# Kernel optimization log

Hardware: AMD Instinct MI355X
Metric: run time of the kernel (lower is better)

## Reference

```python
import jax, jax.numpy as jnp
import numpy as np

E = 20    # number of residue types (rc.restypes)
NB = 2    # num_blocks per AngleHead
NA = 7    # num_angles
C_S = 384
C_H = 128
BS, L = 8, 2048


def setup_inputs() -> dict:
    key = jax.random.key(0)
    ks = jax.random.split(key, 16)
    sc = 0.02
    return {
        "s": jax.random.normal(ks[0], (BS, L, C_S), dtype=jnp.float32),
        "s_init": jax.random.normal(ks[1], (BS, L, C_S), dtype=jnp.float32),
        "aatype": jax.random.randint(ks[2], (BS, L), 0, E, dtype=jnp.int32),
        # stacked per-residue-type AngleHead params
        "Win": jax.random.normal(ks[3], (E, C_S, C_H), dtype=jnp.float32) * sc,
        "b_in": jax.random.normal(ks[4], (E, C_H), dtype=jnp.float32) * sc,
        "Winit": jax.random.normal(ks[5], (E, C_S, C_H), dtype=jnp.float32) * sc,
        "b_init2": jax.random.normal(ks[6], (E, C_H), dtype=jnp.float32) * sc,
        "Wb1": jax.random.normal(ks[7], (E, NB, C_H, C_H), dtype=jnp.float32) * sc,
        "bb1": jax.random.normal(ks[8], (E, NB, C_H), dtype=jnp.float32) * sc,
        "Wb2": jax.random.normal(ks[9], (E, NB, C_H, C_H), dtype=jnp.float32) * sc,
        "bb2": jax.random.normal(ks[10], (E, NB, C_H), dtype=jnp.float32) * sc,
        "Wout": jax.random.normal(ks[11], (E, C_H, NA * 2), dtype=jnp.float32) * sc,
        "b_out": jax.random.normal(ks[12], (E, NA * 2), dtype=jnp.float32) * sc,
    }


def reference(s, s_init, aatype, Win, b_in, Winit, b_init2, Wb1, bb1, Wb2, bb2, Wout, b_out):
    relu = jax.nn.relu
    bs, seq_len, c_s = s.shape
    N = bs * seq_len
    sf = s.reshape(N, c_s)          # [N, c_s]
    si = s_init.reshape(N, c_s)     # [N, c_s]

    # Dense dispatch: run every token through all E per-type heads, then
    # combine with the one-hot routing mask (math identical to the torch
    # gather/scatter loop over residue types).
    h = jnp.einsum('nd,edh->neh', relu(sf), Win) + b_in            # [N,E,H]
    h = h + jnp.einsum('nd,edh->neh', relu(si), Winit) + b_init2   # [N,E,H]

    for b in range(NB):  # ResidualBlock1d: s + W2 @ relu(W1 @ relu(s))
        a = jnp.einsum('neh,ehk->nek', relu(h), Wb1[:, b]) + bb1[:, b]
        a = jnp.einsum('nek,ekh->neh', relu(a), Wb2[:, b]) + bb2[:, b]
        h = h + a

    out = jnp.einsum('neh,eho->neo', relu(h), Wout) + b_out        # [N,E,2*NA]
    sel = jax.nn.one_hot(aatype.reshape(N), E, dtype=out.dtype)    # [N,E]
    ang = jnp.einsum('neo,ne->no', out, sel).reshape(bs, seq_len, NA, 2)

    # F.normalize(dim=-1): x / max(||x||, eps)
    nrm = jnp.maximum(jnp.linalg.norm(ang, axis=-1, keepdims=True), 1e-12)
    return ang / nrm
```

## Files before the change

kernel.cpp:

```cpp
#include <hip/hip_runtime.h>
#include <math.h>

#define E_TYPES 20
#define NBLK 2
#define NANG 7
#define CS 384
#define CH 128
#define N_TOK (8 * 2048)
#define TOK 32
#define TPB 256
#define TPB_MAIN 512
#define KC 128
#define MAX_TILES (N_TOK / TOK + E_TYPES)
#define NPREP 64

#define HIST_OFF 0

#define WT1_OFF (256 * 1024)
#define WT1_SZ  (20 * 8 * 24 * 2048)
#define WTR_OFF (WT1_OFF + WT1_SZ)

typedef __attribute__((ext_vector_type(8))) short bfrag;
typedef __attribute__((ext_vector_type(4))) float f32x4;
typedef unsigned short (*arr136)[136];

#define BAR() do { \
    asm volatile("s_waitcnt lgkmcnt(0)" ::: "memory"); \
    __builtin_amdgcn_s_barrier(); \
    asm volatile("" ::: "memory"); \
} while (0)

__device__ __forceinline__ void split_bf16(float x, unsigned short& h, unsigned short& l) {
    unsigned int u = __float_as_uint(x);
    unsigned int hb = (u + 0x7FFFu + ((u >> 16) & 1u)) & 0xFFFF0000u;
    h = (unsigned short)(hb >> 16);
    float r = x - __uint_as_float(hb);
    unsigned int v = __float_as_uint(r);
    l = (unsigned short)((v + 0x7FFFu + ((v >> 16) & 1u)) >> 16);
}

__global__ void prep1(const float* __restrict__ Win, const float* __restrict__ Winit,
                      const float* __restrict__ Wb1, const float* __restrict__ Wb2,
                      const int* __restrict__ aatype, int* __restrict__ wsI,
                      unsigned short* __restrict__ wt) {
    __shared__ int lh[E_TYPES];
    int bid = blockIdx.x;
    int t = threadIdx.x;
    if (bid >= 1600) {
        int b2 = bid - 1600;
        if (t < E_TYPES) lh[t] = 0;
        __syncthreads();
        int idx = b2 * 256 + t;
        if (idx < N_TOK) atomicAdd(&lh[aatype[idx]], 1);
        __syncthreads();
        if (t < E_TYPES) wsI[HIST_OFF + b2 * E_TYPES + t] = lh[t];
        return;
    }
    int gid = bid * 256 + t;
    unsigned short h[8], l[8];
    if (gid < 245760) {
        int lane = gid & 63;
        int bi = gid >> 6;
        int kb = bi % 24;
        int r = bi / 24;
        int nt = r & 7, e = r >> 3;
        int n = nt * 16 + (lane & 15);
        int k0 = kb * 32 + (lane >> 4) * 8;
        #pragma unroll
        for (int j = 0; j < 8; j++) {
            int k = k0 + j;
            float x = (k < CS) ? Win[((size_t)e * CS + k) * CH + n]
                               : Winit[((size_t)e * CS + (k - CS)) * CH + n];
            split_bf16(x, h[j], l[j]);
        }
        unsigned short* dst = wt + (WT1_OFF / 2) + (size_t)bi * 1024 + lane * 8;
        *(bfrag*)dst = *(bfrag*)h;
        *(bfrag*)(dst + 512) = *(bfrag*)l;
    } else {
        gid -= 245760;
        int lane = gid & 63;
        int bi = gid >> 6;
        int kb = bi & 3;
        int nt = (bi >> 2) & 7;
        int m4 = (bi >> 5) & 3;
        int e = bi >> 7;
        int b = m4 >> 1;
        const float* W = (m4 & 1) ? Wb2 : Wb1;
        int n = nt * 16 + (lane & 15);
        int k0 = kb * 32 + (lane >> 4) * 8;
        #pragma unroll
        for (int j = 0; j < 8; j++) {
            int k = k0 + j;
            float x = W[(((size_t)e * NBLK + b) * CH + k) * CH + n];
            split_bf16(x, h[j], l[j]);
        }
        unsigned short* dst = wt + (WTR_OFF / 2) + (size_t)bi * 1024 + lane * 8;
        *(bfrag*)dst = *(bfrag*)h;
        *(bfrag*)(dst + 512) = *(bfrag*)l;
    }
}

#define MFMA(a, b, c) __builtin_amdgcn_mfma_f32_16x16x32_bf16((a), (b), (c), 0, 0, 0)

__global__ __launch_bounds__(TPB_MAIN, 4)
void angle_main(const float* __restrict__ s, const float* __restrict__ si,
                const float* __restrict__ b_in, const float* __restrict__ b_init2,
                const float* __restrict__ bb1, const float* __restrict__ bb2,
                const float* __restrict__ Wout, const float* __restrict__ b_out,
                const int* __restrict__ aatype,
                const int* __restrict__ wsI, const unsigned short* __restrict__ wt,
                float* __restrict__ out)
{
    #define BUFSZ 17408
    __shared__ __align__(16) char pool[2 * BUFSZ];
    __shared__ int ptok[TOK];
    __shared__ int cntS[E_TYPES];

    arr136 AH0 = (arr136)(pool);
    arr136 AL0 = (arr136)(pool + 8704);
    arr136 AH1 = (arr136)(pool + BUFSZ);
    arr136 AL1 = (arr136)(pool + BUFSZ + 8704);
    float (*Hf)[132] = (float (*)[132])(pool);
    float (*Of)[16]  = (float (*)[16])(pool + BUFSZ);

    int t = threadIdx.x;
    int w = t >> 6, lane = t & 63;
    int lane15 = lane & 15, quad = lane >> 4;

    int bid = blockIdx.x;
    const int q = MAX_TILES >> 3, r = MAX_TILES & 7;
    int xcd = bid & 7, sub = bid >> 3;
    int tile = (xcd < r ? xcd * (q + 1) : r * (q + 1) + (xcd - r) * q) + sub;

    if (w == 0 && lane < E_TYPES) {
        int c = 0;
        #pragma unroll
        for (int b = 0; b < NPREP; b++) c += wsI[HIST_OFF + b * E_TYPES + lane];
        cntS[lane] = c;
    }
    BAR();

    int pos = tile * TOK;
    int e = -1, poff_e = 0;
    {
        int accT = 0;
        #pragma unroll
        for (int ee = 0; ee < E_TYPES; ee++) {
            int pad = (cntS[ee] + TOK - 1) & ~(TOK - 1);
            if (e < 0 && pos < accT + pad) { e = ee; poff_e = accT; }
            accT += pad;
        }
        if (pos >= accT) return;
    }
    int pos_in = pos - poff_e;
    int n = cntS[e] - pos_in; if (n > TOK) n = TOK;

    int nc = w * 16 + lane15;
    const bfrag* wt1 = (const bfrag*)((const char*)wt + WT1_OFF);
    const bfrag* wtr = (const bfrag*)((const char*)wt + WTR_OFF);
    size_t wb = (size_t)(e * 8 + w) * 24;

    bfrag Bd[2][4];
    {
        const bfrag* nb = wt1 + wb * 128 + lane;
        Bd[0][0] = nb[0];   Bd[0][1] = nb[128];
        Bd[0][2] = nb[64];  Bd[0][3] = nb[192];
    }
    float bv_in  = b_in[e * CH + nc] + b_init2[e * CH + nc];
    float bvb1a = bb1[(e * NBLK + 0) * CH + nc];
    float bvb1b = bb1[(e * NBLK + 1) * CH + nc];
    float bvb2a = bb2[(e * NBLK + 0) * CH + nc];
    float bvb2b = bb2[(e * NBLK + 1) * CH + nc];

    if (w == 0) {
        int hb = wsI[HIST_OFF + lane * E_TYPES + e];
        int inc = hb;
        #pragma unroll
        for (int d = 1; d < 64; d <<= 1) { int v = __shfl_up(inc, d); if (lane >= d) inc += v; }
        int pre = inc - hb;
        unsigned long long mle = __ballot(pre <= pos_in);
        int cb = 63 - __clzll(mle);
        int running = __shfl(pre, cb);
        int base = cb * 256;
        int lim = pos_in + n;
        while (running < lim && base < N_TOK) {
            const int4 a4 = *(const int4*)&aatype[base + lane * 4];
            int m0 = (a4.x == e), m1 = (a4.y == e), m2 = (a4.z == e), m3 = (a4.w == e);
            int c = m0 + m1 + m2 + m3;
            int incl = c;
            #pragma unroll
            for (int d = 1; d < 64; d <<= 1) { int v = __shfl_up(incl, d); if (lane >= d) incl += v; }
            int rk = running + incl - c;
            int tk = base + lane * 4;
            if (m0) { if (rk >= pos_in && rk < lim) ptok[rk - pos_in] = tk;     rk++; }
            if (m1) { if (rk >= pos_in && rk < lim) ptok[rk - pos_in] = tk + 1; rk++; }
            if (m2) { if (rk >= pos_in && rk < lim) ptok[rk - pos_in] = tk + 2; rk++; }
            if (m3) { if (rk >= pos_in && rk < lim) ptok[rk - pos_in] = tk + 3; rk++; }
            running += __shfl(incl, 63);
            base += 256;
        }
        int t0 = ptok[0];
        if (lane >= n && lane < TOK) ptok[lane] = t0;
    }
    BAR();

    int srow = t >> 4;
    int scol = (t & 15) * 8;
    size_t rowoff = (size_t)ptok[srow] * CS + scol;
    float4 p0 = *(const float4*)(s + rowoff);
    float4 p1 = *(const float4*)(s + rowoff + 4);
    {
        float xv[8] = {p0.x, p0.y, p0.z, p0.w, p1.x, p1.y, p1.z, p1.w};
        unsigned short h8[8], l8[8];
        #pragma unroll
        for (int j = 0; j < 8; j++) split_bf16(fmaxf(xv[j], 0.f), h8[j], l8[j]);
        *(bfrag*)&AH0[srow][scol] = *(bfrag*)h8;
        *(bfrag*)&AL0[srow][scol] = *(bfrag*)l8;
    }
    p0 = *(const float4*)(s + rowoff + KC);
    p1 = *(const float4*)(s + rowoff + KC + 4);

    f32x4 aA0 = (f32x4){bv_in, bv_in, bv_in, bv_in};
    f32x4 aA1 = aA0;
    f32x4 aB0 = (f32x4){0.f, 0.f, 0.f, 0.f};
    f32x4 aB1 = aB0;
    BAR();

    #pragma unroll
    for (int c = 0; c < 6; c++) {
        arr136 WAH = (c & 1) ? AH1 : AH0;
        arr136 WAL = (c & 1) ? AL1 : AL0;
        const bfrag* wbase = wt1 + (wb + c * 4) * 128 + lane;
        bfrag c2h = wbase[256], c2l = wbase[320];
        bfrag c3h = wbase[384], c3l = wbase[448];
        #pragma unroll
        for (int ks = 0; ks < 4; ks++) {
            bfrag bh = (ks == 0) ? Bd[c & 1][0] : (ks == 1) ? Bd[c & 1][1]
                      : (ks == 2) ? c2h : c3h;
            bfrag bl = (ks == 0) ? Bd[c & 1][2] : (ks == 1) ? Bd[c & 1][3]
                      : (ks == 2) ? c2l : c3l;
            int kl = ks * 32 + quad * 8;
            bfrag ah0 = *(const bfrag*)&WAH[lane15][kl];
            bfrag ah1 = *(const bfrag*)&WAH[16 + lane15][kl];
            bfrag al0 = *(const bfrag*)&WAL[lane15][kl];
            bfrag al1 = *(const bfrag*)&WAL[16 + lane15][kl];
            aA0 = MFMA(ah0, bh, aA0);
            aB0 = MFMA(ah0, bl, aB0);
            aB0 = MFMA(al0, bh, aB0);
            aA1 = MFMA(ah1, bh, aA1);
            aB1 = MFMA(ah1, bl, aB1);
            aB1 = MFMA(al1, bh, aB1);
            if (ks == 1) {
                const bfrag* nb = (c < 5)
                    ? wt1 + (wb + (c + 1) * 4) * 128 + lane
                    : wtr + ((size_t)(e * 4 + 0) * 8 + w) * 4 * 128 + lane;
                Bd[(c + 1) & 1][0] = nb[0];   Bd[(c + 1) & 1][1] = nb[128];
                Bd[(c + 1) & 1][2] = nb[64];  Bd[(c + 1) & 1][3] = nb[192];
            }
        }
        if (c < 5) {
            arr136 NH = (c & 1) ? AH0 : AH1;
            arr136 NL = (c & 1) ? AL0 : AL1;
            float xv[8] = {p0.x, p0.y, p0.z, p0.w, p1.x, p1.y, p1.z, p1.w};
            unsigned short h8[8], l8[8];
            #pragma unroll
            for (int j = 0; j < 8; j++) split_bf16(fmaxf(xv[j], 0.f), h8[j], l8[j]);
            *(bfrag*)&NH[srow][scol] = *(bfrag*)h8;
            *(bfrag*)&NL[srow][scol] = *(bfrag*)l8;
            if (c < 4) {
                const float* src = (c + 2 < 3) ? s : si;
                int kb0 = ((c + 2 < 3) ? (c + 2) : (c - 1)) * KC;
                p0 = *(const float4*)(src + rowoff + kb0);
                p1 = *(const float4*)(src + rowoff + kb0 + 4);
            }
        }
        BAR();
    }

    f32x4 h0 = aA0 + aB0;
    f32x4 h1 = aA1 + aB1;
    {
        f32x4 cur[2] = {h0, h1};
        #pragma unroll
        for (int mt = 0; mt < 2; mt++) {
            #pragma unroll
            for (int rr = 0; rr < 4; rr++) {
                unsigned short hh, ll;
                split_bf16(fmaxf(cur[mt][rr], 0.f), hh, ll);
                AH0[mt * 16 + quad * 4 + rr][nc] = hh;
                AL0[mt * 16 + quad * 4 + rr][nc] = ll;
            }
        }
    }
    BAR();

    #pragma unroll
    for (int g = 0; g < 4; g++) {
        arr136 WAH = (g & 1) ? AH1 : AH0;
        arr136 WAL = (g & 1) ? AL1 : AL0;
        const bfrag* wbase = wtr + ((size_t)(e * 4 + g) * 8 + w) * 4 * 128 + lane;
        bfrag c2h = wbase[256], c2l = wbase[320];
        bfrag c3h = wbase[384], c3l = wbase[448];
        float bv = (g & 1) ? ((g >> 1) ? bvb2b : bvb2a)
                           : ((g >> 1) ? bvb1b : bvb1a);
        f32x4 rA0 = (f32x4){bv, bv, bv, bv}, rA1 = rA0;
        f32x4 rB0 = (f32x4){0.f, 0.f, 0.f, 0.f}, rB1 = rB0;
        #pragma unroll
        for (int ks = 0; ks < 4; ks++) {
            bfrag bh = (ks == 0) ? Bd[g & 1][0] : (ks == 1) ? Bd[g & 1][1]
                      : (ks == 2) ? c2h : c3h;
            bfrag bl = (ks == 0) ? Bd[g & 1][2] : (ks == 1) ? Bd[g & 1][3]
                      : (ks == 2) ? c2l : c3l;
            int kl = ks * 32 + quad * 8;
            bfrag ah0 = *(const bfrag*)&WAH[lane15][kl];
            bfrag ah1 = *(const bfrag*)&WAH[16 + lane15][kl];
            bfrag al0 = *(const bfrag*)&WAL[lane15][kl];
            bfrag al1 = *(const bfrag*)&WAL[16 + lane15][kl];
            rA0 = MFMA(ah0, bh, rA0);
            rB0 = MFMA(ah0, bl, rB0);
            rB0 = MFMA(al0, bh, rB0);
            rA1 = MFMA(ah1, bh, rA1);
            rB1 = MFMA(ah1, bl, rB1);
            rB1 = MFMA(al1, bh, rB1);
            if (ks == 1 && g < 3) {
                const bfrag* nb = wtr + ((size_t)(e * 4 + g + 1) * 8 + w) * 4 * 128 + lane;
                Bd[(g + 1) & 1][0] = nb[0];   Bd[(g + 1) & 1][1] = nb[128];
                Bd[(g + 1) & 1][2] = nb[64];  Bd[(g + 1) & 1][3] = nb[192];
            }
        }
        f32x4 r0 = rA0 + rB0, r1 = rA1 + rB1;
        if (g & 1) { h0 += r0; h1 += r1; }
        if (g < 3) {
            f32x4 cur0 = (g & 1) ? h0 : r0;
            f32x4 cur1 = (g & 1) ? h1 : r1;
            arr136 NH = (g & 1) ? AH0 : AH1;
            arr136 NL = (g & 1) ? AL0 : AL1;
            #pragma unroll
            for (int rr = 0; rr < 4; rr++) {
                unsigned short hh, ll;
                split_bf16(fmaxf(cur0[rr], 0.f), hh, ll);
                NH[quad * 4 + rr][nc] = hh;
                NL[quad * 4 + rr][nc] = ll;
                split_bf16(fmaxf(cur1[rr], 0.f), hh, ll);
                NH[16 + quad * 4 + rr][nc] = hh;
                NL[16 + quad * 4 + rr][nc] = ll;
            }
            BAR();
        } else {
            #pragma unroll
            for (int rr = 0; rr < 4; rr++) {
                Hf[quad * 4 + rr][nc]      = fmaxf(h0[rr], 0.f);
                Hf[16 + quad * 4 + rr][nc] = fmaxf(h1[rr], 0.f);
            }
            BAR();
        }
    }

    const float* WoutE = Wout + (size_t)e * CH * (NANG * 2);
    const float* boutE = b_out + (size_t)e * (NANG * 2);
    for (int idx = t; idx < n * (NANG * 2); idx += TPB_MAIN) {
        int i = idx / (NANG * 2);
        int o = idx - i * (NANG * 2);
        float v0 = boutE[o], v1 = 0.f, v2 = 0.f, v3 = 0.f;
        #pragma unroll 4
        for (int k = 0; k < CH; k += 4) {
            v0 = fmaf(Hf[i][k],     WoutE[(size_t)k * (NANG * 2) + o],       v0);
            v1 = fmaf(Hf[i][k + 1], WoutE[(size_t)(k + 1) * (NANG * 2) + o], v1);
            v2 = fmaf(Hf[i][k + 2], WoutE[(size_t)(k + 2) * (NANG * 2) + o], v2);
            v3 = fmaf(Hf[i][k + 3], WoutE[(size_t)(k + 3) * (NANG * 2) + o], v3);
        }
        Of[i][o] = (v0 + v1) + (v2 + v3);
    }
    BAR();

    for (int idx = t; idx < n * NANG; idx += TPB_MAIN) {
        int i = idx / NANG;
        int a = idx - i * NANG;
        float x = Of[i][2 * a];
        float y = Of[i][2 * a + 1];
        float nr = fmaxf(sqrtf(x * x + y * y), 1e-12f);
        size_t base = (size_t)ptok[i] * (NANG * 2) + 2 * a;
        out[base]     = x / nr;
        out[base + 1] = y / nr;
    }
}

extern "C" void kernel_launch(void* const* d_in, const int* in_sizes, int n_in,
                              void* d_out, int out_size, void* d_ws, size_t ws_size,
                              hipStream_t stream) {
    const float* s       = (const float*)d_in[0];
    const float* s_init  = (const float*)d_in[1];
    const int*   aatype  = (const int*)d_in[2];
    const float* Win     = (const float*)d_in[3];
    const float* b_in    = (const float*)d_in[4];
    const float* Winit   = (const float*)d_in[5];
    const float* b_init2 = (const float*)d_in[6];
    const float* Wb1     = (const float*)d_in[7];
    const float* bb1     = (const float*)d_in[8];
    const float* Wb2     = (const float*)d_in[9];
    const float* bb2     = (const float*)d_in[10];
    const float* Wout    = (const float*)d_in[11];
    const float* b_out   = (const float*)d_in[12];
    int* wsI = (int*)d_ws;
    unsigned short* wt = (unsigned short*)d_ws;
    float* out = (float*)d_out;

    hipLaunchKernelGGL(prep1, dim3(1664), dim3(256), 0, stream,
                       Win, Winit, Wb1, Wb2, aatype, wsI, wt);
    hipLaunchKernelGGL(angle_main, dim3(MAX_TILES), dim3(TPB_MAIN), 0, stream,
                       s, s_init, b_in, b_init2, bb1, bb2, Wout, b_out,
                       aatype, wsI, wt, out);
}
```

Measured before the change: 161.0 us.

## Halve token tile to 16 rows and restructure staging into a single buffer per chunk

Shrinks the per-block token tile from 32 to 16, so each wave computes one 16-row MFMA tile instead of two and per-type padding waste is smaller. Shared memory buffers are halved, and input staging now loads one float4 per thread per chunk and writes it into the current buffer before a barrier, rather than prefetching into the alternate buffer. The custom barrier macro is replaced with __syncthreads and the occupancy hint is dropped from launch bounds. The cost is twice as many blocks, so every block re-reads the per-type weights, and it adds an extra barrier per chunk with less overlap between loads and MFMA work.

New measurement: 159.4 us. Within noise of the previous version (-1.0%).

```diff
diff --git a/kernel.cpp b/kernel.cpp
--- a/kernel.cpp
+++ b/kernel.cpp
@@ -7,7 +7,7 @@
 #define CS 384
 #define CH 128
 #define N_TOK (8 * 2048)
-#define TOK 32
+#define TOK 16
 #define TPB 256
 #define TPB_MAIN 512
 #define KC 128
@@ -23,12 +23,6 @@
 typedef __attribute__((ext_vector_type(8))) short bfrag;
 typedef __attribute__((ext_vector_type(4))) float f32x4;
 typedef unsigned short (*arr136)[136];
-
-#define BAR() do { \
-    asm volatile("s_waitcnt lgkmcnt(0)" ::: "memory"); \
-    __builtin_amdgcn_s_barrier(); \
-    asm volatile("" ::: "memory"); \
-} while (0)
 
 __device__ __forceinline__ void split_bf16(float x, unsigned short& h, unsigned short& l) {
     unsigned int u = __float_as_uint(x);
@@ -102,7 +96,7 @@
 
 #define MFMA(a, b, c) __builtin_amdgcn_mfma_f32_16x16x32_bf16((a), (b), (c), 0, 0, 0)
 
-__global__ __launch_bounds__(TPB_MAIN, 4)
+__global__ __launch_bounds__(TPB_MAIN)
 void angle_main(const float* __restrict__ s, const float* __restrict__ si,
                 const float* __restrict__ b_in, const float* __restrict__ b_init2,
                 const float* __restrict__ bb1, const float* __restrict__ bb2,
@@ -111,15 +105,15 @@
                 const int* __restrict__ wsI, const unsigned short* __restrict__ wt,
                 float* __restrict__ out)
 {
-    #define BUFSZ 17408
+    #define BUFSZ 8704
     __shared__ __align__(16) char pool[2 * BUFSZ];
     __shared__ int ptok[TOK];
     __shared__ int cntS[E_TYPES];
 
     arr136 AH0 = (arr136)(pool);
-    arr136 AL0 = (arr136)(pool + 8704);
+    arr136 AL0 = (arr136)(pool + 4352);
     arr136 AH1 = (arr136)(pool + BUFSZ);
-    arr136 AL1 = (arr136)(pool + BUFSZ + 8704);
+    arr136 AL1 = (arr136)(pool + BUFSZ + 4352);
     float (*Hf)[132] = (float (*)[132])(pool);
     float (*Of)[16]  = (float (*)[16])(pool + BUFSZ);
 
@@ -138,7 +132,7 @@
         for (int b = 0; b < NPREP; b++) c += wsI[HIST_OFF + b * E_TYPES + lane];
         cntS[lane] = c;
     }
-    BAR();
+    __syncthreads();
 
     int pos = tile * TOK;
     int e = -1, poff_e = 0;
@@ -202,34 +196,35 @@
         int t0 = ptok[0];
         if (lane >= n && lane < TOK) ptok[lane] = t0;
     }
-    BAR();
-
-    int srow = t >> 4;
-    int scol = (t & 15) * 8;
+    __syncthreads();
+
+    int srow = t >> 5;
+    int scol = (t & 31) * 4;
     size_t rowoff = (size_t)ptok[srow] * CS + scol;
     float4 p0 = *(const float4*)(s + rowoff);
-    float4 p1 = *(const float4*)(s + rowoff + 4);
-    {
-        float xv[8] = {p0.x, p0.y, p0.z, p0.w, p1.x, p1.y, p1.z, p1.w};
-        unsigned short h8[8], l8[8];
-        #pragma unroll
-        for (int j = 0; j < 8; j++) split_bf16(fmaxf(xv[j], 0.f), h8[j], l8[j]);
-        *(bfrag*)&AH0[srow][scol] = *(bfrag*)h8;
-        *(bfrag*)&AL0[srow][scol] = *(bfrag*)l8;
-    }
-    p0 = *(const float4*)(s + rowoff + KC);
-    p1 = *(const float4*)(s + rowoff + KC + 4);
-
-    f32x4 aA0 = (f32x4){bv_in, bv_in, bv_in, bv_in};
-    f32x4 aA1 = aA0;
-    f32x4 aB0 = (f32x4){0.f, 0.f, 0.f, 0.f};
-    f32x4 aB1 = aB0;
-    BAR();
+
+    f32x4 aA = (f32x4){bv_in, bv_in, bv_in, bv_in};
+    f32x4 aB = (f32x4){0.f, 0.f, 0.f, 0.f};
 
     #pragma unroll
     for (int c = 0; c < 6; c++) {
         arr136 WAH = (c & 1) ? AH1 : AH0;
         arr136 WAL = (c & 1) ? AL1 : AL0;
+        {
+            ushort4 hv, lv;
+            split_bf16(fmaxf(p0.x, 0.f), hv.x, lv.x);
+            split_bf16(fmaxf(p0.y, 0.f), hv.y, lv.y);
+            split_bf16(fmaxf(p0.z, 0.f), hv.z, lv.z);
+            split_bf16(fmaxf(p0.w, 0.f), hv.w, lv.w);
+            *(ushort4*)&WAH[srow][scol] = hv;
+            *(ushort4*)&WAL[srow][scol] = lv;
+        }
+        if (c < 5) {
+            const float* src = (c + 1 < 3) ? s : si;
+            int kb0 = ((c + 1 < 3) ? (c + 1) : (c - 2)) * KC;
+            p0 = *(const float4*)(src + rowoff + kb0);
+        }
+        __syncthreads();
         const bfrag* wbase = wt1 + (wb + c * 4) * 128 + lane;
         bfrag c2h = wbase[256], c2l = wbase[320];
         bfrag c3h = wbase[384], c3l = wbase[448];
@@ -240,16 +235,11 @@
             bfrag bl = (ks == 0) ? Bd[c & 1][2] : (ks == 1) ? Bd[c & 1][3]
                       : (ks == 2) ? c2l : c3l;
             int kl = ks * 32 + quad * 8;
-            bfrag ah0 = *(const bfrag*)&WAH[lane15][kl];
-            bfrag ah1 = *(const bfrag*)&WAH[16 + lane15][kl];
-            bfrag al0 = *(const bfrag*)&WAL[lane15][kl];
-            bfrag al1 = *(const bfrag*)&WAL[16 + lane15][kl];
-            aA0 = MFMA(ah0, bh, aA0);
-            aB0 = MFMA(ah0, bl, aB0);
-            aB0 = MFMA(al0, bh, aB0);
-            aA1 = MFMA(ah1, bh, aA1);
-            aB1 = MFMA(ah1, bl, aB1);
-            aB1 = MFMA(al1, bh, aB1);
+            bfrag ah = *(const bfrag*)&WAH[lane15][kl];
+            bfrag al = *(const bfrag*)&WAL[lane15][kl];
+            aA = MFMA(ah, bh, aA);
+            aB = MFMA(ah, bl, aB);
+            aB = MFMA(al, bh, aB);
             if (ks == 1) {
                 const bfrag* nb = (c < 5)
                     ? wt1 + (wb + (c + 1) * 4) * 128 + lane
@@ -258,41 +248,20 @@
                 Bd[(c + 1) & 1][2] = nb[64];  Bd[(c + 1) & 1][3] = nb[192];
             }
         }
-        if (c < 5) {
-            arr136 NH = (c & 1) ? AH0 : AH1;
-            arr136 NL = (c & 1) ? AL0 : AL1;
-            float xv[8] = {p0.x, p0.y, p0.z, p0.w, p1.x, p1.y, p1.z, p1.w};
-            unsigned short h8[8], l8[8];
-            #pragma unroll
-            for (int j = 0; j < 8; j++) split_bf16(fmaxf(xv[j], 0.f), h8[j], l8[j]);
-            *(bfrag*)&NH[srow][scol] = *(bfrag*)h8;
-            *(bfrag*)&NL[srow][scol] = *(bfrag*)l8;
-            if (c < 4) {
-                const float* src = (c + 2 < 3) ? s : si;
-                int kb0 = ((c + 2 < 3) ? (c + 2) : (c - 1)) * KC;
-                p0 = *(const float4*)(src + rowoff + kb0);
-                p1 = *(const float4*)(src + rowoff + kb0 + 4);
-            }
-        }
-        BAR();
-    }
-
-    f32x4 h0 = aA0 + aB0;
-    f32x4 h1 = aA1 + aB1;
+        __syncthreads();
+    }
+
+    f32x4 h0 = aA + aB;
     {
-        f32x4 cur[2] = {h0, h1};
-        #pragma unroll
-        for (int mt = 0; mt < 2; mt++) {
-            #pragma unroll
-            for (int rr = 0; rr < 4; rr++) {
-                unsigned short hh, ll;
-                split_bf16(fmaxf(cur[mt][rr], 0.f), hh, ll);
-                AH0[mt * 16 + quad * 4 + rr][nc] = hh;
-                AL0[mt * 16 + quad * 4 + rr][nc] = ll;
-            }
-        }
-    }
-    BAR();
+        #pragma unroll
+        for (int rr = 0; rr < 4; rr++) {
+            unsigned short hh, ll;
+            split_bf16(fmaxf(h0[rr], 0.f), hh, ll);
+            AH0[quad * 4 + rr][nc] = hh;
+            AL0[quad * 4 + rr][nc] = ll;
+        }
+    }
+    __syncthreads();
 
     #pragma unroll
     for (int g = 0; g < 4; g++) {
@@ -303,8 +272,8 @@
         bfrag c3h = wbase[384], c3l = wbase[448];
         float bv = (g & 1) ? ((g >> 1) ? bvb2b : bvb2a)
                            : ((g >> 1) ? bvb1b : bvb1a);
-        f32x4 rA0 = (f32x4){bv, bv, bv, bv}, rA1 = rA0;
-        f32x4 rB0 = (f32x4){0.f, 0.f, 0.f, 0.f}, rB1 = rB0;
+        f32x4 rA = (f32x4){bv, bv, bv, bv};
+        f32x4 rB = (f32x4){0.f, 0.f, 0.f, 0.f};
         #pragma unroll
         for (int ks = 0; ks < 4; ks++) {
             bfrag bh = (ks == 0) ? Bd[g & 1][0] : (ks == 1) ? Bd[g & 1][1]
@@ -312,47 +281,36 @@
             bfrag bl = (ks == 0) ? Bd[g & 1][2] : (ks == 1) ? Bd[g & 1][3]
                       : (ks == 2) ? c2l : c3l;
             int kl = ks * 32 + quad * 8;
-            bfrag ah0 = *(const bfrag*)&WAH[lane15][kl];
-            bfrag ah1 = *(const bfrag*)&WAH[16 + lane15][kl];
-            bfrag al0 = *(const bfrag*)&WAL[lane15][kl];
-            bfrag al1 = *(const bfrag*)&WAL[16 + lane15][kl];
-            rA0 = MFMA(ah0, bh, rA0);
-            rB0 = MFMA(ah0, bl, rB0);
-            rB0 = MFMA(al0, bh, rB0);
-            rA1 = MFMA(ah1, bh, rA1);
-            rB1 = MFMA(ah1, bl, rB1);
-            rB1 = MFMA(al1, bh, rB1);
+            bfrag ah = *(const bfrag*)&WAH[lane15][kl];
+            bfrag al = *(const bfrag*)&WAL[lane15][kl];
+            rA = MFMA(ah, bh, rA);
+            rB = MFMA(ah, bl, rB);
+            rB = MFMA(al, bh, rB);
             if (ks == 1 && g < 3) {
                 const bfrag* nb = wtr + ((size_t)(e * 4 + g + 1) * 8 + w) * 4 * 128 + lane;
                 Bd[(g + 1) & 1][0] = nb[0];   Bd[(g + 1) & 1][1] = nb[128];
                 Bd[(g + 1) & 1][2] = nb[64];  Bd[(g + 1) & 1][3] = nb[192];
             }
         }
-        f32x4 r0 = rA0 + rB0, r1 = rA1 + rB1;
-        if (g & 1) { h0 += r0; h1 += r1; }
+        f32x4 r0 = rA + rB;
+        if (g & 1) h0 += r0;
         if (g < 3) {
-            f32x4 cur0 = (g & 1) ? h0 : r0;
-            f32x4 cur1 = (g & 1) ? h1 : r1;
+            f32x4 cur = (g & 1) ? h0 : r0;
             arr136 NH = (g & 1) ? AH0 : AH1;
             arr136 NL = (g & 1) ? AL0 : AL1;
             #pragma unroll
             for (int rr = 0; rr < 4; rr++) {
                 unsigned short hh, ll;
-                split_bf16(fmaxf(cur0[rr], 0.f), hh, ll);
+                split_bf16(fmaxf(cur[rr], 0.f), hh, ll);
                 NH[quad * 4 + rr][nc] = hh;
                 NL[quad * 4 + rr][nc] = ll;
-                split_bf16(fmaxf(cur1[rr], 0.f), hh, ll);
-                NH[16 + quad * 4 + rr][nc] = hh;
-                NL[16 + quad * 4 + rr][nc] = ll;
             }
-            BAR();
+            __syncthreads();
         } else {
             #pragma unroll
-            for (int rr = 0; rr < 4; rr++) {
-                Hf[quad * 4 + rr][nc]      = fmaxf(h0[rr], 0.f);
-                Hf[16 + quad * 4 + rr][nc] = fmaxf(h1[rr], 0.f);
-            }
-            BAR();
+            for (int rr = 0; rr < 4; rr++)
+                Hf[quad * 4 + rr][nc] = fmaxf(h0[rr], 0.f);
+            __syncthreads();
         }
     }
 
@@ -371,7 +329,7 @@
         }
         Of[i][o] = (v0 + v1) + (v2 + v3);
     }
-    BAR();
+    __syncthreads();
 
     for (int idx = t; idx < n * NANG; idx += TPB_MAIN) {
         int i = idx / NANG;
```
